# Performance work log

Measured on AMD Instinct MI355X. Metric: run time of the kernel, lower is better.

## Reference

```python
import jax, jax.numpy as jnp
import numpy as np

B, T, D, E, H, K = 4, 2048, 1024, 8, 2048, 2


def setup_inputs() -> dict:
    key = jax.random.key(0)
    k0, k1, k2, k3 = jax.random.split(key, 4)
    x = jax.random.normal(k0, (B, T, D), dtype=jnp.float32)
    router_w = jax.random.normal(k1, (E, D), dtype=jnp.float32) * (D ** -0.5)
    w1 = jax.random.normal(k2, (E, D, H), dtype=jnp.float32) * (D ** -0.5)
    w2 = jax.random.normal(k3, (E, H, D), dtype=jnp.float32) * (H ** -0.5)
    return {"x": x, "router_w": router_w, "w1": w1, "w2": w2}


def reference(x, router_w, w1, w2):
    Bb, Tt, Dd = x.shape
    N = Bb * Tt
    # --- router: top-k selection + renormalized softmax weights ---
    logits = jnp.einsum('btd,ed->bte', x, router_w)            # [B,T,E]
    top_vals, top_idx = jax.lax.top_k(logits, K)               # [B,T,K]
    top_w = jax.nn.softmax(top_vals, axis=-1)                  # [B,T,K]
    # --- dense per-expert FFN (relu-squared activation) ---
    xf = x.reshape(N, Dd)                                      # [N,D]
    h = jnp.einsum('nd,edh->enh', xf, w1)                      # [E,N,H]
    h = jnp.square(jax.nn.relu(h))
    y = jnp.einsum('enh,ehd->end', h, w2)                      # [E,N,D]
    # --- gather selected experts and combine ---
    idx_f = top_idx.reshape(N, K)                              # [N,K]
    w_f = top_w.reshape(N, K)                                  # [N,K]
    y_sel = y[idx_f, jnp.arange(N)[:, None]]                   # [N,K,D]
    out = jnp.einsum('nk,nkd->nd', w_f, y_sel)                 # [N,D]
    return out.reshape(Bb, Tt, Dd)
```

## Files before the change

### kernel.cpp

```cpp
#include <hip/hip_runtime.h>
#include <hip/hip_bf16.h>
#include <stdint.h>

#define ND    1024
#define NE    8
#define NH    2048
#define NTOK  8192
#define NPAIR (NTOK*2)

typedef unsigned short u16;
typedef __attribute__((ext_vector_type(8))) short bf16x8;
typedef __attribute__((ext_vector_type(4))) float f32x4;

__device__ __forceinline__ u16 f2bf(float f) {
    union { float f; unsigned u; } v; v.f = f;
    return (u16)((v.u + 0x7fffu + ((v.u >> 16) & 1u)) >> 16);
}

__device__ __forceinline__ void gl_lds16(const void* g, void* l) {
    __builtin_amdgcn_global_load_lds(
        (const __attribute__((address_space(1))) unsigned int*)g,
        (__attribute__((address_space(3))) unsigned int*)l, 16, 0, 0);
}

#define CTRL_OFFS  16
#define CTRL_BC    32
#define CTRL_BB    288
#define CTRL_TOPK  544

__global__ __launch_bounds__(256) void router_topk2(
    const float* __restrict__ x, const float* __restrict__ rw,
    int* __restrict__ topk_idx, float* __restrict__ topk_w)
{
    const int n    = blockIdx.x * 4 + (threadIdx.x >> 6);
    const int lane = threadIdx.x & 63;
    const float* xr = x + (size_t)n * ND;
    float4 xv[4];
    #pragma unroll
    for (int i = 0; i < 4; ++i) xv[i] = *(const float4*)(xr + lane*16 + i*4);

    float lg[NE];
    #pragma unroll
    for (int e = 0; e < NE; ++e) {
        const float* wr_ = rw + (size_t)e * ND + lane*16;
        float a = 0.f;
        #pragma unroll
        for (int i = 0; i < 4; ++i) {
            float4 wv = *(const float4*)(wr_ + i*4);
            a += xv[i].x*wv.x + xv[i].y*wv.y + xv[i].z*wv.z + xv[i].w*wv.w;
        }
        #pragma unroll
        for (int s = 32; s; s >>= 1) a += __shfl_xor(a, s);
        lg[e] = a;
    }
    if (lane == 0) {
        int i0 = 0; float v0 = lg[0];
        #pragma unroll
        for (int i = 1; i < NE; ++i) { float v = lg[i]; if (v > v0) { v0 = v; i0 = i; } }
        int i1 = -1; float v1 = -3.4e38f;
        #pragma unroll
        for (int i = 0; i < NE; ++i) {
            if (i == i0) continue;
            float v = lg[i]; if (v > v1) { v1 = v; i1 = i; }
        }
        float w0 = 1.f / (1.f + expf(v1 - v0));
        topk_idx[n*2]   = i0;  topk_idx[n*2+1] = i1;
        topk_w [n*2]    = w0;  topk_w [n*2+1]  = 1.f - w0;
    }
}

__global__ __launch_bounds__(256) void hist_blocks(
    const int* __restrict__ topk_idx, int* __restrict__ blockcounts)
{
    __shared__ int c[NE];
    const int tid = threadIdx.x;
    if (tid < NE) c[tid] = 0;
    __syncthreads();
    const int n = blockIdx.x * 256 + tid;
    atomicAdd(&c[topk_idx[n*2]],   1);
    atomicAdd(&c[topk_idx[n*2+1]], 1);
    __syncthreads();
    if (tid < NE) blockcounts[blockIdx.x * NE + tid] = c[tid];
}

__global__ void prefix2(int* __restrict__ ctrl)
{
    const int e = threadIdx.x;
    const int* bc = ctrl + CTRL_BC;
    int* offsets  = ctrl + CTRL_OFFS;
    int* bbase    = ctrl + CTRL_BB;
    if (e < NE) {
        int run = 0;
        int tmp[32];
        #pragma unroll
        for (int b = 0; b < 32; ++b) { tmp[b] = run; run += bc[b*NE + e]; }
        int total = run, pre = 0;
        #pragma unroll
        for (int i = 0; i < NE; ++i) {
            int v = __shfl(total, i);
            if (i < e) pre += v;
        }
        offsets[e] = pre;
        if (e == NE-1) offsets[NE] = pre + total;
        #pragma unroll
        for (int b = 0; b < 32; ++b) bbase[b*NE + e] = pre + tmp[b];
    }
}

__global__ __launch_bounds__(256) void scatter2(
    const int* __restrict__ topk_idx, const float* __restrict__ topk_w,
    const int* __restrict__ ctrl,
    int* __restrict__ bucket_tok, float* __restrict__ bucket_gw)
{
    __shared__ int wc[4][NE];
    const int b = blockIdx.x, tid = threadIdx.x;
    const int w = tid >> 6, l = tid & 63;
    const int n = b*256 + tid;
    const int e0 = topk_idx[n*2], e1 = topk_idx[n*2+1];
    const unsigned long long lt = (1ULL << l) - 1ULL;

    int rank0 = 0, rank1 = 0;
    #pragma unroll
    for (int e = 0; e < NE; ++e) {
        unsigned long long m0 = __ballot(e0 == e);
        unsigned long long m1 = __ballot(e1 == e);
        int c0 = __popcll(m0);
        if (e0 == e) rank0 = __popcll(m0 & lt);
        if (e1 == e) rank1 = c0 + __popcll(m1 & lt);
        if (l == 0) wc[w][e] = c0 + __popcll(m1);
    }
    __syncthreads();
    const int* bbase = ctrl + CTRL_BB;
    int wo0 = 0, wo1 = 0;
    #pragma unroll
    for (int w2 = 0; w2 < 4; ++w2) {
        if (w2 < w) { wo0 += wc[w2][e0]; wo1 += wc[w2][e1]; }
    }
    int p0 = bbase[b*NE + e0] + wo0 + rank0;
    int p1 = bbase[b*NE + e1] + wo1 + rank1;
    bucket_tok[p0] = n;  bucket_gw[p0] = topk_w[n*2];
    bucket_tok[p1] = n;  bucket_gw[p1] = topk_w[n*2+1];
}

__global__ __launch_bounds__(256) void transpose_cvt(
    const float* __restrict__ src, u16* __restrict__ dst, int R, int C)
{
    __shared__ float tb[64][65];
    const int tpc = C >> 6;
    const int tr = blockIdx.x / tpc;
    const int tc = blockIdx.x % tpc;
    src += (size_t)blockIdx.y * R * C;
    dst += (size_t)blockIdx.y * R * C;
    const int tid = threadIdx.x;
    #pragma unroll
    for (int i = 0; i < 4; ++i) {
        int idx = i*256 + tid;
        int r = idx >> 4, c4 = (idx & 15) * 4;
        float4 v = *(const float4*)(src + (size_t)(tr*64 + r)*C + tc*64 + c4);
        tb[r][c4] = v.x; tb[r][c4+1] = v.y; tb[r][c4+2] = v.z; tb[r][c4+3] = v.w;
    }
    __syncthreads();
    #pragma unroll
    for (int i = 0; i < 2; ++i) {
        int idx = i*256 + tid;
        int c = idx >> 3, s8 = (idx & 7) * 8;
        union { u16 u[8]; uint4 v; } pk;
        #pragma unroll
        for (int j = 0; j < 8; ++j) pk.u[j] = f2bf(tb[s8 + j][c]);
        *(uint4*)(dst + (size_t)(tc*64 + c)*R + tr*64 + s8) = pk.v;
    }
}

__global__ __launch_bounds__(256) void gather_cvt(
    const float* __restrict__ x, const int* __restrict__ bucket_tok, u16* __restrict__ Xg)
{
    const int pair = blockIdx.x * 4 + (threadIdx.x >> 6);
    const int lane = threadIdx.x & 63;
    const float* xr = x + (size_t)bucket_tok[pair] * ND;
    u16* dr = Xg + (size_t)pair * ND;
    const int d0 = lane * 16;
    float4 a = *(const float4*)(xr + d0);
    float4 b = *(const float4*)(xr + d0 + 4);
    float4 c = *(const float4*)(xr + d0 + 8);
    float4 d = *(const float4*)(xr + d0 + 12);
    union { u16 u[8]; uint4 v; } p0, p1;
    p0.u[0]=f2bf(a.x); p0.u[1]=f2bf(a.y); p0.u[2]=f2bf(a.z); p0.u[3]=f2bf(a.w);
    p0.u[4]=f2bf(b.x); p0.u[5]=f2bf(b.y); p0.u[6]=f2bf(b.z); p0.u[7]=f2bf(b.w);
    p1.u[0]=f2bf(c.x); p1.u[1]=f2bf(c.y); p1.u[2]=f2bf(c.z); p1.u[3]=f2bf(c.w);
    p1.u[4]=f2bf(d.x); p1.u[5]=f2bf(d.y); p1.u[6]=f2bf(d.z); p1.u[7]=f2bf(d.w);
    *(uint4*)(dr + d0)     = p0.v;
    *(uint4*)(dr + d0 + 8) = p1.v;
}

template<int KSTEPS, int EPI, int NT_TILES, int WPE_SHIFT>
__global__ __launch_bounds__(256, 2) void pass_gemm(
    const u16* __restrict__ Amat, const u16* __restrict__ Bmat,
    const int* __restrict__ bucket_tok, const float* __restrict__ bucket_gw,
    const int* __restrict__ ctrl,
    u16* __restrict__ A1out, float* __restrict__ out)
{
    const int K   = KSTEPS * 64;
    const int bid = blockIdx.x;
    const int w   = ((bid & 7) << WPE_SHIFT) | (bid >> 3);
    const int e   = w >> WPE_SHIFT;
    const int r   = w & ((1 << WPE_SHIFT) - 1);
    const int nt0 = (r % NT_TILES) * 128;
    const int mt0 = (r / NT_TILES) * 128;
    const int* offsets = ctrl + CTRL_OFFS;
    const int beg = offsets[e];
    const int cnt = offsets[e+1] - beg;
    if (mt0 >= cnt) return;

    extern __shared__ u16 sm[];

    const int tid  = threadIdx.x;
    const int wv   = tid >> 6;
    const int lane = tid & 63;
    const int l15  = lane & 15;
    const int grp  = lane >> 4;
    const int wr   = wv >> 1, wc = wv & 1;
    const int rmax = cnt - mt0 - 1;

    const u16* Abase = Amat + (size_t)beg * K;
    const u16* Bb    = Bmat + (size_t)e * NH * ND;

    const int rsub  = lane >> 3;
    const int csrc0 = lane & 7;

    auto stage = [&](int buf, int kt) {
        #pragma unroll
        for (int c = 0; c < 4; ++c) {
            int row = c*32 + wv*8 + rsub;
            int chunk = csrc0 ^ (row & 7);
            int lrow = row > rmax ? rmax : row;
            const u16* ga = Abase + (size_t)(mt0 + lrow) * K + kt*64 + chunk*8;
            gl_lds16(ga, sm + buf*8192 + c*2048 + wv*512);
            const u16* gb = Bb + (size_t)(nt0 + row) * K + kt*64 + chunk*8;
            gl_lds16(gb, sm + 16384 + buf*8192 + c*2048 + wv*512);
        }
    };

    f32x4 acc[4][4];
    #pragma unroll
    for (int mt = 0; mt < 4; ++mt)
        #pragma unroll
        for (int nt = 0; nt < 4; ++nt) acc[mt][nt] = 0;

    stage(0, 0);
    int cur = 0;
    for (int kt = 0; kt < KSTEPS; ++kt) {
        __syncthreads();
        if (kt + 1 < KSTEPS) stage(cur ^ 1, kt + 1);
        const char* As = (const char*)(sm + cur*8192);
        const char* Bs = (const char*)(sm + 16384 + cur*8192);
        #pragma unroll
        for (int kk = 0; kk < 2; ++kk) {
            bf16x8 af[4], bfr[4];
            #pragma unroll
            for (int mt = 0; mt < 4; ++mt) {
                int row = wr*64 + mt*16 + l15;
                int kb  = ((kk*32 + grp*8)*2) ^ ((row & 7) << 4);
                af[mt] = *(const bf16x8*)(As + row*128 + kb);
            }
            #pragma unroll
            for (int nt = 0; nt < 4; ++nt) {
                int row = wc*64 + nt*16 + l15;
                int kb  = ((kk*32 + grp*8)*2) ^ ((row & 7) << 4);
                bfr[nt] = *(const bf16x8*)(Bs + row*128 + kb);
            }
            #pragma unroll
            for (int mt = 0; mt < 4; ++mt)
                #pragma unroll
                for (int nt = 0; nt < 4; ++nt)
                    acc[mt][nt] = __builtin_amdgcn_mfma_f32_16x16x32_bf16(af[mt], bfr[nt], acc[mt][nt], 0,0,0);
        }
        cur ^= 1;
    }

    #pragma unroll
    for (int mt = 0; mt < 4; ++mt) {
        #pragma unroll
        for (int r4 = 0; r4 < 4; ++r4) {
            int ml = mt0 + wr*64 + mt*16 + grp*4 + r4;
            if (ml >= cnt) continue;
            if (EPI == 0) {
                u16* dst = A1out + (size_t)(beg + ml) * NH + nt0 + wc*64 + l15;
                #pragma unroll
                for (int nt = 0; nt < 4; ++nt) {
                    float v = fmaxf(acc[mt][nt][r4], 0.f);
                    dst[nt*16] = f2bf(v * v);
                }
            } else {
                int   p = bucket_tok[beg + ml];
                float g = bucket_gw [beg + ml];
                float* orow = out + (size_t)p * ND + nt0 + wc*64 + l15;
                #pragma unroll
                for (int nt = 0; nt < 4; ++nt)
                    atomicAdd(orow + nt*16, g * acc[mt][nt][r4]);
            }
        }
    }
}

extern "C" void kernel_launch(void* const* d_in, const int* in_sizes, int n_in,
                              void* d_out, int out_size, void* d_ws, size_t ws_size,
                              hipStream_t stream) {
    const float* x  = (const float*)d_in[0];
    const float* rw = (const float*)d_in[1];
    const float* w1 = (const float*)d_in[2];
    const float* w2 = (const float*)d_in[3];
    float* out = (float*)d_out;

    int*   ctrl        = (int*)d_ws;
    int*   blockcounts = ctrl + CTRL_BC;
    int*   topk_idx    = ctrl + CTRL_TOPK;
    float* topk_w      = (float*)(topk_idx + NPAIR);
    int*   bucket_tok  = (int*)(topk_w + NPAIR);
    float* bucket_gw   = (float*)(bucket_tok + NPAIR);

    const size_t CTRL_BYTES = (size_t)1 << 19;
    const size_t WT_BYTES   = (size_t)NE * NH * ND * sizeof(u16);

    hipMemsetAsync(d_out, 0, (size_t)NTOK * ND * sizeof(float), stream);

    router_topk2<<<NTOK/4, 256, 0, stream>>>(x, rw, topk_idx, topk_w);
    hist_blocks<<<NTOK/256, 256, 0, stream>>>(topk_idx, blockcounts);
    prefix2<<<1, 64, 0, stream>>>(ctrl);
    scatter2<<<NTOK/256, 256, 0, stream>>>(topk_idx, topk_w, ctrl, bucket_tok, bucket_gw);

    u16* w1t = (u16*)((char*)d_ws + CTRL_BYTES);
    u16* shr = (u16*)((char*)d_ws + CTRL_BYTES + WT_BYTES);
    u16* A1  = (u16*)((char*)d_ws + CTRL_BYTES + 2*WT_BYTES);

    transpose_cvt<<<dim3(512, NE), 256, 0, stream>>>(w1, w1t, ND, NH);
    gather_cvt<<<NPAIR/4, 256, 0, stream>>>(x, bucket_tok, shr);

    pass_gemm<16, 0, 16, 11><<<8 << 11, 256, 65536, stream>>>(
        shr, w1t, bucket_tok, bucket_gw, ctrl, A1, nullptr);

    transpose_cvt<<<dim3(512, NE), 256, 0, stream>>>(w2, shr, NH, ND);

    pass_gemm<32, 1, 8, 10><<<8 << 10, 256, 65536, stream>>>(
        A1, shr, bucket_tok, bucket_gw, ctrl, nullptr, out);
}
```

Measured before the change: 290.1 us.

## Use 256x128 tiles with 512 threads and triple-buffered async LDS pipeline

The grouped GEMM moves to 512-thread blocks computing 256-row by 128-column tiles, so each B tile is reused across twice as many rows. It also replaces the double buffer and per-step __syncthreads with a three-stage ring buffer that prefetches two k-steps ahead, using explicit vmcnt waits plus a raw barrier. The aim is to cut B-operand traffic and hide global-to-LDS latency. In exchange it uses 144KB of LDS per block, which forces one block per CU, and relies on precise vmcnt counting being correct.

```diff
diff --git a/kernel.cpp b/kernel.cpp
--- a/kernel.cpp
+++ b/kernel.cpp
@@ -193,7 +193,7 @@
 }
 
 template<int KSTEPS, int EPI, int NT_TILES, int WPE_SHIFT>
-__global__ __launch_bounds__(256, 2) void pass_gemm(
+__global__ __launch_bounds__(512, 1) void pass_gemm(
     const u16* __restrict__ Amat, const u16* __restrict__ Bmat,
     const int* __restrict__ bucket_tok, const float* __restrict__ bucket_gw,
     const int* __restrict__ ctrl,
@@ -205,7 +205,7 @@
     const int e   = w >> WPE_SHIFT;
     const int r   = w & ((1 << WPE_SHIFT) - 1);
     const int nt0 = (r % NT_TILES) * 128;
-    const int mt0 = (r / NT_TILES) * 128;
+    const int mt0 = (r / NT_TILES) * 256;
     const int* offsets = ctrl + CTRL_OFFS;
     const int beg = offsets[e];
     const int cnt = offsets[e+1] - beg;
@@ -218,25 +218,33 @@
     const int lane = tid & 63;
     const int l15  = lane & 15;
     const int grp  = lane >> 4;
-    const int wr   = wv >> 1, wc = wv & 1;
+    const int wr   = wv >> 1;
+    const int wc   = wv & 1;
     const int rmax = cnt - mt0 - 1;
 
     const u16* Abase = Amat + (size_t)beg * K;
     const u16* Bb    = Bmat + (size_t)e * NH * ND;
 
-    const int rsub  = lane >> 3;
-    const int csrc0 = lane & 7;
+    const int rsub8 = lane >> 3;
+    const int cs    = lane & 7;
 
     auto stage = [&](int buf, int kt) {
+        u16* bA = sm + buf * 24576;
+        u16* bB = bA + 16384;
         #pragma unroll
         for (int c = 0; c < 4; ++c) {
-            int row = c*32 + wv*8 + rsub;
-            int chunk = csrc0 ^ (row & 7);
-            int lrow = row > rmax ? rmax : row;
+            int row   = wv*32 + c*8 + rsub8;
+            int chunk = cs ^ (row & 7);
+            int lrow  = row > rmax ? rmax : row;
             const u16* ga = Abase + (size_t)(mt0 + lrow) * K + kt*64 + chunk*8;
-            gl_lds16(ga, sm + buf*8192 + c*2048 + wv*512);
+            gl_lds16(ga, bA + wv*2048 + c*512);
+        }
+        #pragma unroll
+        for (int c = 0; c < 2; ++c) {
+            int row   = wv*16 + c*8 + rsub8;
+            int chunk = cs ^ (row & 7);
             const u16* gb = Bb + (size_t)(nt0 + row) * K + kt*64 + chunk*8;
-            gl_lds16(gb, sm + 16384 + buf*8192 + c*2048 + wv*512);
+            gl_lds16(gb, bB + wv*1024 + c*512);
         }
     };
 
@@ -247,12 +255,19 @@
         for (int nt = 0; nt < 4; ++nt) acc[mt][nt] = 0;
 
     stage(0, 0);
-    int cur = 0;
+    stage(1, 1);
+    int bcur = 0;
     for (int kt = 0; kt < KSTEPS; ++kt) {
-        __syncthreads();
-        if (kt + 1 < KSTEPS) stage(cur ^ 1, kt + 1);
-        const char* As = (const char*)(sm + cur*8192);
-        const char* Bs = (const char*)(sm + 16384 + cur*8192);
+        if (kt + 1 < KSTEPS) { asm volatile("s_waitcnt vmcnt(6)" ::: "memory"); }
+        else                 { asm volatile("s_waitcnt vmcnt(0)" ::: "memory"); }
+        __builtin_amdgcn_s_barrier();
+        __builtin_amdgcn_sched_barrier(0);
+        if (kt + 2 < KSTEPS) {
+            int bnx = bcur + 2; if (bnx >= 3) bnx -= 3;
+            stage(bnx, kt + 2);
+        }
+        const char* As = (const char*)(sm + bcur * 24576);
+        const char* Bs = (const char*)(sm + bcur * 24576 + 16384);
         #pragma unroll
         for (int kk = 0; kk < 2; ++kk) {
             bf16x8 af[4], bfr[4];
@@ -274,7 +289,7 @@
                 for (int nt = 0; nt < 4; ++nt)
                     acc[mt][nt] = __builtin_amdgcn_mfma_f32_16x16x32_bf16(af[mt], bfr[nt], acc[mt][nt], 0,0,0);
         }
-        cur ^= 1;
+        bcur = (bcur == 2) ? 0 : bcur + 1;
     }
 
     #pragma unroll
@@ -335,11 +350,13 @@
     transpose_cvt<<<dim3(512, NE), 256, 0, stream>>>(w1, w1t, ND, NH);
     gather_cvt<<<NPAIR/4, 256, 0, stream>>>(x, bucket_tok, shr);
 
-    pass_gemm<16, 0, 16, 11><<<8 << 11, 256, 65536, stream>>>(
+    const size_t shbytes = 3 * 24576 * sizeof(u16);
+
+    pass_gemm<16, 0, 16, 10><<<8 << 10, 512, shbytes, stream>>>(
         shr, w1t, bucket_tok, bucket_gw, ctrl, A1, nullptr);
 
     transpose_cvt<<<dim3(512, NE), 256, 0, stream>>>(w2, shr, NH, ND);
 
-    pass_gemm<32, 1, 8, 10><<<8 << 10, 256, 65536, stream>>>(
+    pass_gemm<32, 1, 8, 9><<<8 << 9, 512, shbytes, stream>>>(
         A1, shr, bucket_tok, bucket_gw, ctrl, nullptr, out);
 }
```

After: 336.0 us. 1.16x slower.

## Use 256x128 GEMM tiles with a 32-wide K step

Applied to the files above, without the earlier changes.

Changes the grouped expert GEMM tile from 128x128 with a K step of 64 to 256x128 with a K step of 32. Each wave now computes 128x64 outputs using 32 accumulators, and the LDS swizzle becomes a 4-chunk XOR. The shared-memory footprint drops to 48KB, and the grid halves because each block covers twice as many rows. B-tile reuse per load rises, but the change doubles the number of K iterations and syncs, raises register pressure, and wastes more work on partially filled expert tiles.

```diff
diff --git a/kernel.cpp b/kernel.cpp
--- a/kernel.cpp
+++ b/kernel.cpp
@@ -199,13 +199,13 @@
     const int* __restrict__ ctrl,
     u16* __restrict__ A1out, float* __restrict__ out)
 {
-    const int K   = KSTEPS * 64;
+    const int K   = KSTEPS * 32;
     const int bid = blockIdx.x;
     const int w   = ((bid & 7) << WPE_SHIFT) | (bid >> 3);
     const int e   = w >> WPE_SHIFT;
     const int r   = w & ((1 << WPE_SHIFT) - 1);
     const int nt0 = (r % NT_TILES) * 128;
-    const int mt0 = (r / NT_TILES) * 128;
+    const int mt0 = (r / NT_TILES) * 256;
     const int* offsets = ctrl + CTRL_OFFS;
     const int beg = offsets[e];
     const int cnt = offsets[e+1] - beg;
@@ -218,31 +218,39 @@
     const int lane = tid & 63;
     const int l15  = lane & 15;
     const int grp  = lane >> 4;
-    const int wr   = wv >> 1, wc = wv & 1;
+    const int wr   = wv >> 1;
+    const int wc   = wv & 1;
     const int rmax = cnt - mt0 - 1;
 
     const u16* Abase = Amat + (size_t)beg * K;
     const u16* Bb    = Bmat + (size_t)e * NH * ND;
 
-    const int rsub  = lane >> 3;
-    const int csrc0 = lane & 7;
+    const int lrow16 = lane >> 2;
+    const int lchunk = lane & 3;
 
     auto stage = [&](int buf, int kt) {
+        u16* bA = sm + buf * 12288;
+        u16* bB = bA + 8192;
         #pragma unroll
         for (int c = 0; c < 4; ++c) {
-            int row = c*32 + wv*8 + rsub;
-            int chunk = csrc0 ^ (row & 7);
-            int lrow = row > rmax ? rmax : row;
-            const u16* ga = Abase + (size_t)(mt0 + lrow) * K + kt*64 + chunk*8;
-            gl_lds16(ga, sm + buf*8192 + c*2048 + wv*512);
-            const u16* gb = Bb + (size_t)(nt0 + row) * K + kt*64 + chunk*8;
-            gl_lds16(gb, sm + 16384 + buf*8192 + c*2048 + wv*512);
+            int row   = wv*64 + c*16 + lrow16;
+            int chunk = lchunk ^ (row & 3);
+            int lrow  = row > rmax ? rmax : row;
+            const u16* ga = Abase + (size_t)(mt0 + lrow) * K + kt*32 + chunk*8;
+            gl_lds16(ga, bA + wv*2048 + c*512);
+        }
+        #pragma unroll
+        for (int c = 0; c < 2; ++c) {
+            int row   = wv*32 + c*16 + lrow16;
+            int chunk = lchunk ^ (row & 3);
+            const u16* gb = Bb + (size_t)(nt0 + row) * K + kt*32 + chunk*8;
+            gl_lds16(gb, bB + wv*1024 + c*512);
         }
     };
 
-    f32x4 acc[4][4];
-    #pragma unroll
-    for (int mt = 0; mt < 4; ++mt)
+    f32x4 acc[8][4];
+    #pragma unroll
+    for (int mt = 0; mt < 8; ++mt)
         #pragma unroll
         for (int nt = 0; nt < 4; ++nt) acc[mt][nt] = 0;
 
@@ -251,37 +259,35 @@
     for (int kt = 0; kt < KSTEPS; ++kt) {
         __syncthreads();
         if (kt + 1 < KSTEPS) stage(cur ^ 1, kt + 1);
-        const char* As = (const char*)(sm + cur*8192);
-        const char* Bs = (const char*)(sm + 16384 + cur*8192);
-        #pragma unroll
-        for (int kk = 0; kk < 2; ++kk) {
-            bf16x8 af[4], bfr[4];
+        const char* As = (const char*)(sm + cur * 12288);
+        const char* Bs = As + 16384;
+
+        bf16x8 af[8], bfr[4];
+        #pragma unroll
+        for (int nt = 0; nt < 4; ++nt) {
+            int row = wc*64 + nt*16 + l15;
+            int kb  = (grp ^ (row & 3)) << 4;
+            bfr[nt] = *(const bf16x8*)(Bs + row*64 + kb);
+        }
+        #pragma unroll
+        for (int mt = 0; mt < 8; ++mt) {
+            int row = wr*128 + mt*16 + l15;
+            int kb  = (grp ^ (row & 3)) << 4;
+            af[mt] = *(const bf16x8*)(As + row*64 + kb);
+        }
+        #pragma unroll
+        for (int mt = 0; mt < 8; ++mt)
             #pragma unroll
-            for (int mt = 0; mt < 4; ++mt) {
-                int row = wr*64 + mt*16 + l15;
-                int kb  = ((kk*32 + grp*8)*2) ^ ((row & 7) << 4);
-                af[mt] = *(const bf16x8*)(As + row*128 + kb);
-            }
-            #pragma unroll
-            for (int nt = 0; nt < 4; ++nt) {
-                int row = wc*64 + nt*16 + l15;
-                int kb  = ((kk*32 + grp*8)*2) ^ ((row & 7) << 4);
-                bfr[nt] = *(const bf16x8*)(Bs + row*128 + kb);
-            }
-            #pragma unroll
-            for (int mt = 0; mt < 4; ++mt)
-                #pragma unroll
-                for (int nt = 0; nt < 4; ++nt)
-                    acc[mt][nt] = __builtin_amdgcn_mfma_f32_16x16x32_bf16(af[mt], bfr[nt], acc[mt][nt], 0,0,0);
-        }
+            for (int nt = 0; nt < 4; ++nt)
+                acc[mt][nt] = __builtin_amdgcn_mfma_f32_16x16x32_bf16(af[mt], bfr[nt], acc[mt][nt], 0,0,0);
         cur ^= 1;
     }
 
     #pragma unroll
-    for (int mt = 0; mt < 4; ++mt) {
+    for (int mt = 0; mt < 8; ++mt) {
         #pragma unroll
         for (int r4 = 0; r4 < 4; ++r4) {
-            int ml = mt0 + wr*64 + mt*16 + grp*4 + r4;
+            int ml = mt0 + wr*128 + mt*16 + grp*4 + r4;
             if (ml >= cnt) continue;
             if (EPI == 0) {
                 u16* dst = A1out + (size_t)(beg + ml) * NH + nt0 + wc*64 + l15;
@@ -335,11 +341,13 @@
     transpose_cvt<<<dim3(512, NE), 256, 0, stream>>>(w1, w1t, ND, NH);
     gather_cvt<<<NPAIR/4, 256, 0, stream>>>(x, bucket_tok, shr);
 
-    pass_gemm<16, 0, 16, 11><<<8 << 11, 256, 65536, stream>>>(
+    const size_t shbytes = 2 * 12288 * sizeof(u16);
+
+    pass_gemm<32, 0, 16, 10><<<8 << 10, 256, shbytes, stream>>>(
         shr, w1t, bucket_tok, bucket_gw, ctrl, A1, nullptr);
 
     transpose_cvt<<<dim3(512, NE), 256, 0, stream>>>(w2, shr, NH, ND);
 
-    pass_gemm<32, 1, 8, 10><<<8 << 10, 256, 65536, stream>>>(
+    pass_gemm<64, 1, 8, 9><<<8 << 9, 256, shbytes, stream>>>(
         A1, shr, bucket_tok, bucket_gw, ctrl, nullptr, out);
 }
```

New measurement: 334.0 us. 1.15x slower.
